# Optimization experiments

Measured on AMD Instinct MI355X. Metric: run time of the kernel, lower is better.

## Reference

```python
import jax, jax.numpy as jnp
import numpy as np

F_SIZE = 256
N_HEAD = 4
D_HEAD = F_SIZE // N_HEAD
B = 16384
E = 31  # number of 'other' entities


def setup_inputs() -> dict:
    key = jax.random.key(0)
    ks = jax.random.split(key, 9)
    s = 1.0 / np.sqrt(F_SIZE)  # ~ nn.Linear init scale
    inp = {
        "ego": jax.random.normal(ks[0], (B, 1, F_SIZE), dtype=jnp.float32),
        "others": jax.random.normal(ks[1], (B, E, F_SIZE), dtype=jnp.float32),
        "mask": jax.random.randint(ks[2], (B, E + 1), 0, 2).astype(bool),
        "Wq": jax.random.uniform(ks[3], (F_SIZE, F_SIZE), jnp.float32, -s, s),
        "Wk": jax.random.uniform(ks[4], (F_SIZE, F_SIZE), jnp.float32, -s, s),
        "Wv": jax.random.uniform(ks[5], (F_SIZE, F_SIZE), jnp.float32, -s, s),
        "Wok": jax.random.uniform(ks[6], (F_SIZE, F_SIZE), jnp.float32, -s, s),
        "Wov": jax.random.uniform(ks[7], (F_SIZE, F_SIZE), jnp.float32, -s, s),
        "Wc": jax.random.uniform(ks[8], (F_SIZE, F_SIZE), jnp.float32, -s, s),
    }
    return inp


def reference(ego, others, mask, Wq, Wk, Wv, Wok, Wov, Wc):
    b = others.shape[0]
    e = others.shape[1]
    # nn.Linear(bias=False): y = x @ W.T
    ego_q = (ego @ Wq.T).reshape(b, 1, N_HEAD, D_HEAD)
    ego_k = (ego @ Wk.T).reshape(b, 1, N_HEAD, D_HEAD)
    ego_v = (ego @ Wv.T).reshape(b, 1, N_HEAD, D_HEAD)
    oth_k = (others @ Wok.T).reshape(b, e, N_HEAD, D_HEAD)
    oth_v = (others @ Wov.T).reshape(b, e, N_HEAD, D_HEAD)
    all_k = jnp.concatenate([ego_k, oth_k], axis=1)  # (b, e+1, h, d)
    all_v = jnp.concatenate([ego_v, oth_v], axis=1)
    # scores: single query per head -> (b, h, 1, e+1)
    scores = jnp.einsum('bqhd,bkhd->bhqk', ego_q, all_k) / np.sqrt(D_HEAD)
    scores = jnp.where(mask[:, None, None, :], jnp.float32(-1e9), scores)
    attn = jax.nn.softmax(scores, axis=-1)
    value = jnp.einsum('bhqk,bkhd->bqhd', attn, all_v).reshape(b, F_SIZE)
    res = ((value @ Wc.T) + ego[:, 0, :]) * 0.5
    return res, attn
```

## Files before the change

kernel.cpp:

```cpp
#include <hip/hip_runtime.h>
#include <hip/hip_bf16.h>

typedef __attribute__((ext_vector_type(8))) short bf16x8;
typedef __attribute__((ext_vector_type(4))) float f32x4;

#define NB 16384
#define NE 31

static __device__ __forceinline__ unsigned short f2b(float f) {
  unsigned int u = __builtin_bit_cast(unsigned int, f);
  return (unsigned short)((u + 0x7fffu + ((u >> 16) & 1u)) >> 16);
}
static __device__ __forceinline__ float b2f(unsigned short h) {
  return __builtin_bit_cast(float, ((unsigned int)h) << 16);
}
static __device__ __forceinline__ unsigned int cvtpk(float a, float b) {
  unsigned int r;
  asm("v_cvt_pk_bf16_f32 %0, %1, %2" : "=v"(r) : "v"(a), "v"(b));
  return r;
}

__global__ void k0_all(const float* __restrict__ wq, const float* __restrict__ wk,
                       const float* __restrict__ wv, const float* __restrict__ wok,
                       const float* __restrict__ wov, const float* __restrict__ wc,
                       unsigned short* __restrict__ W1, unsigned short* __restrict__ W2) {
  int r = blockIdx.x, k = threadIdx.x;
  if (r < 1024) {
    if (r < 256) {
      W1[r * 256 + k] = f2b(0.125f * wq[r * 256 + k]);
    } else if (r < 512) {
      W1[r * 256 + k] = f2b(wk[(r - 256) * 256 + k]);
    } else if (r < 768) {
      W1[r * 256 + k] = f2b(wv[(r - 512) * 256 + k]);
    } else {
      int n = r - 768;
      W2[n * 1280 + 1024 + k] = f2b(wc[n * 256 + k]);
    }
  } else if (r < 2048) {
    int m = r - 1024;
    int h = m >> 8, c = m & 255;
    float acc = 0.f;
#pragma unroll 8
    for (int d = 0; d < 64; ++d)
      acc = fmaf(wq[(h * 64 + d) * 256 + k], wok[(h * 64 + d) * 256 + c], acc);
    W1[(768 + m) * 256 + k] = f2b(0.125f * acc);
  } else {
    int n = r - 2048;
#pragma unroll 1
    for (int mi = 0; mi < 4; ++mi) {
      float acc = 0.f;
#pragma unroll 8
      for (int d = 0; d < 64; ++d)
        acc = fmaf(wov[(mi * 64 + d) * 256 + k], wc[n * 256 + mi * 64 + d], acc);
      W2[n * 1280 + mi * 256 + k] = f2b(acc);
    }
  }
}

__global__ __launch_bounds__(256, 2)
void k1b(const float* __restrict__ ego, const unsigned short* __restrict__ W1,
         unsigned short* __restrict__ qkv2) {
  __shared__ __align__(16) unsigned short Al[64 * 256];
  const int tid = threadIdx.x;
  const int bM = (blockIdx.x >> 1) * 64;
  const int half = (blockIdx.x & 1) * 896;
#pragma unroll
  for (int it = 0; it < 8; ++it) {
    int c = tid + it * 256;
    int row = c >> 5, k8 = c & 31;
    const float4* g = (const float4*)(ego + (size_t)(bM + row) * 256 + k8 * 8);
    float4 x = g[0], y = g[1];
    float t[8] = {x.x, x.y, x.z, x.w, y.x, y.y, y.z, y.w};
    bf16x8 v;
#pragma unroll
    for (int j = 0; j < 8; ++j) v[j] = (short)f2b(t[j]);
    int byteoff = row * 512 + ((k8 * 16) ^ ((row & 7) << 4));
    *(bf16x8*)((char*)Al + byteoff) = v;
  }
  __syncthreads();
  const int w = tid >> 6, lane = tid & 63, lr = lane & 15, lkg = lane >> 4;
#pragma unroll 1
  for (int cb = 0; cb < 7; ++cb) {
    int bN = half + w * 224 + cb * 32;
    f32x4 acc[4][2];
#pragma unroll
    for (int mt = 0; mt < 4; ++mt)
#pragma unroll
      for (int nt = 0; nt < 2; ++nt) acc[mt][nt] = (f32x4){0.f, 0.f, 0.f, 0.f};
#pragma unroll
    for (int kk = 0; kk < 8; ++kk) {
      int kidx = kk * 32 + lkg * 8;
      bf16x8 bfr[2];
#pragma unroll
      for (int nt = 0; nt < 2; ++nt)
        bfr[nt] = *(const bf16x8*)(W1 + (size_t)(bN + nt * 16 + lr) * 256 + kidx);
#pragma unroll
      for (int mt = 0; mt < 4; ++mt) {
        int row = mt * 16 + lr;
        int byteoff = row * 512 + ((kidx * 2) ^ ((row & 7) << 4));
        bf16x8 a = *(const bf16x8*)((const char*)Al + byteoff);
#pragma unroll
        for (int nt = 0; nt < 2; ++nt)
          acc[mt][nt] = __builtin_amdgcn_mfma_f32_16x16x32_bf16(a, bfr[nt], acc[mt][nt], 0, 0, 0);
      }
    }
#pragma unroll
    for (int mt = 0; mt < 4; ++mt)
#pragma unroll
      for (int nt = 0; nt < 2; ++nt)
#pragma unroll
        for (int j = 0; j < 4; ++j) {
          int row = bM + mt * 16 + lkg * 4 + j;
          int col = bN + nt * 16 + lr;
          qkv2[(size_t)row * 1792 + col] = f2b(acc[mt][nt][j]);
        }
  }
}

__global__ __launch_bounds__(64, 4)
void ks_attn(const float* __restrict__ others, const int* __restrict__ mask,
             const unsigned short* __restrict__ qkv2,
             unsigned short* __restrict__ u,
             float* __restrict__ attnout) {
  __shared__ __align__(16) unsigned short Xs[8192];
  const int lane = threadIdx.x;
  const int lr = lane & 15, lkg = lane >> 4;
  const size_t b = blockIdx.x;
  char* Xc = (char*)Xs;
  const unsigned short* qk = qkv2 + b * 1792;

  bf16x8 af[8];
#pragma unroll
  for (int kk = 0; kk < 8; ++kk)
    af[kk] = *(const bf16x8*)(qk + 768 + (lr & 3) * 256 + kk * 32 + lkg * 8);
  ushort4 qa = *(const ushort4*)(qk + lkg * 64 + lr * 4);
  ushort4 kb = *(const ushort4*)(qk + 256 + lkg * 64 + lr * 4);
  ushort4 ve = *(const ushort4*)(qk + 512 + lane * 4);
  int mk0 = mask[b * 32 + 1 + lr];
  int mk1 = (lr == 15) ? 1 : mask[b * 32 + 17 + lr];
  int mkE = mask[b * 32];

  {
    const char* src = (const char*)(others + b * (NE * 256)) + lane * 16;
#pragma unroll
    for (int j = 0; j < NE; ++j) {
      float4 f = *(const float4*)(src + j * 1024);
      uint2 v;
      v.x = cvtpk(f.x, f.y);
      v.y = cvtpk(f.z, f.w);
      *(uint2*)(Xc + j * 512 + ((lane * 8) ^ ((j & 15) << 4))) = v;
    }
    uint2 z; z.x = 0; z.y = 0;
    *(uint2*)(Xc + 31 * 512 + ((lane * 8) ^ ((31 & 15) << 4))) = z;
  }

  float s0p = b2f(qa.x) * b2f(kb.x) + b2f(qa.y) * b2f(kb.y) +
              b2f(qa.z) * b2f(kb.z) + b2f(qa.w) * b2f(kb.w);
#pragma unroll
  for (int off = 1; off < 16; off <<= 1) s0p += __shfl_xor(s0p, off, 16);
  float s0h[4];
  s0h[0] = __shfl(s0p, 0);
  s0h[1] = __shfl(s0p, 16);
  s0h[2] = __shfl(s0p, 32);
  s0h[3] = __shfl(s0p, 48);

  asm volatile("s_waitcnt lgkmcnt(0)" ::: "memory");
  __builtin_amdgcn_sched_barrier(0);

  f32x4 acc0 = (f32x4){0.f, 0.f, 0.f, 0.f};
  f32x4 acc1 = (f32x4){0.f, 0.f, 0.f, 0.f};
#pragma unroll
  for (int kk = 0; kk < 8; ++kk) {
    int co = kk * 64 + lkg * 16;
    bf16x8 b0 = *(const bf16x8*)(Xc + lr * 512 + (co ^ (lr << 4)));
    bf16x8 b1 = *(const bf16x8*)(Xc + (16 + lr) * 512 + (co ^ (lr << 4)));
    acc0 = __builtin_amdgcn_mfma_f32_16x16x32_bf16(af[kk], b0, acc0, 0, 0, 0);
    acc1 = __builtin_amdgcn_mfma_f32_16x16x32_bf16(af[kk], b1, acc1, 0, 0, 0);
  }

  float pr0[4], pr1[4], p0v[4];
#pragma unroll
  for (int j = 0; j < 4; ++j) {
    float sj0 = mk0 ? -1e9f : acc0[j];
    float sj1 = mk1 ? -1e9f : acc1[j];
    float se  = mkE ? -1e9f : s0h[j];
    float mx = fmaxf(se, fmaxf(sj0, sj1));
#pragma unroll
    for (int off = 1; off < 16; off <<= 1) mx = fmaxf(mx, __shfl_xor(mx, off, 16));
    float e0 = __expf(sj0 - mx), e1 = __expf(sj1 - mx), ee = __expf(se - mx);
    float sm = e0 + e1;
#pragma unroll
    for (int off = 1; off < 16; off <<= 1) sm += __shfl_xor(sm, off, 16);
    float rinv = 1.f / (sm + ee);
    pr0[j] = e0 * rinv;
    pr1[j] = e1 * rinv;
    p0v[j] = ee * rinv;
  }
  if (lkg == 0) {
#pragma unroll
    for (int j = 0; j < 4; ++j) {
      attnout[b * 128 + j * 32 + 1 + lr] = pr0[j];
      if (lr < 15) attnout[b * 128 + j * 32 + 17 + lr] = pr1[j];
      if (lr == 0) attnout[b * 128 + j * 32] = p0v[j];
    }
  }

  f32x4 cx[4];
#pragma unroll
  for (int h = 0; h < 4; ++h) cx[h] = (f32x4){0.f, 0.f, 0.f, 0.f};
#pragma unroll
  for (int e = 0; e < NE; ++e) {
    float p0, p1, p2, p3;
    if (e < 16) {
      p0 = __shfl(pr0[0], e); p1 = __shfl(pr0[1], e);
      p2 = __shfl(pr0[2], e); p3 = __shfl(pr0[3], e);
    } else {
      p0 = __shfl(pr1[0], e - 16); p1 = __shfl(pr1[1], e - 16);
      p2 = __shfl(pr1[2], e - 16); p3 = __shfl(pr1[3], e - 16);
    }
    ushort4 xr = *(const ushort4*)(Xc + e * 512 + ((lane * 8) ^ ((e & 15) << 4)));
    float x0 = b2f(xr.x), x1 = b2f(xr.y), x2 = b2f(xr.z), x3 = b2f(xr.w);
    cx[0][0] = fmaf(p0, x0, cx[0][0]); cx[0][1] = fmaf(p0, x1, cx[0][1]);
    cx[0][2] = fmaf(p0, x2, cx[0][2]); cx[0][3] = fmaf(p0, x3, cx[0][3]);
    cx[1][0] = fmaf(p1, x0, cx[1][0]); cx[1][1] = fmaf(p1, x1, cx[1][1]);
    cx[1][2] = fmaf(p1, x2, cx[1][2]); cx[1][3] = fmaf(p1, x3, cx[1][3]);
    cx[2][0] = fmaf(p2, x0, cx[2][0]); cx[2][1] = fmaf(p2, x1, cx[2][1]);
    cx[2][2] = fmaf(p2, x2, cx[2][2]); cx[2][3] = fmaf(p2, x3, cx[2][3]);
    cx[3][0] = fmaf(p3, x0, cx[3][0]); cx[3][1] = fmaf(p3, x1, cx[3][1]);
    cx[3][2] = fmaf(p3, x2, cx[3][2]); cx[3][3] = fmaf(p3, x3, cx[3][3]);
  }
#pragma unroll
  for (int h = 0; h < 4; ++h) {
    ushort4 st;
    st.x = f2b(cx[h][0]); st.y = f2b(cx[h][1]);
    st.z = f2b(cx[h][2]); st.w = f2b(cx[h][3]);
    *(ushort4*)(u + b * 1280 + h * 256 + lane * 4) = st;
  }
  {
    float p0h = (lkg == 0) ? p0v[0] : (lkg == 1) ? p0v[1] : (lkg == 2) ? p0v[2] : p0v[3];
    ushort4 sv;
    sv.x = f2b(p0h * b2f(ve.x)); sv.y = f2b(p0h * b2f(ve.y));
    sv.z = f2b(p0h * b2f(ve.z)); sv.w = f2b(p0h * b2f(ve.w));
    *(ushort4*)(u + b * 1280 + 1024 + lane * 4) = sv;
  }
}

__global__ __launch_bounds__(256, 2)
void k4_out(const unsigned short* __restrict__ u, const unsigned short* __restrict__ W2,
            const float* __restrict__ ego, float* __restrict__ out) {
  __shared__ __align__(16) unsigned short Au[32 * 256];
  const int tid = threadIdx.x;
  const int bM = blockIdx.x * 32;
  const int w = tid >> 6, lane = tid & 63, lr = lane & 15, lkg = lane >> 4;
  f32x4 acc[2][4];
#pragma unroll
  for (int mt = 0; mt < 2; ++mt)
#pragma unroll
    for (int nt = 0; nt < 4; ++nt) acc[mt][nt] = (f32x4){0.f, 0.f, 0.f, 0.f};
#pragma unroll 1
  for (int kc = 0; kc < 5; ++kc) {
#pragma unroll
    for (int it = 0; it < 4; ++it) {
      int c = tid + it * 256;
      int row = c >> 5, k8 = c & 31;
      bf16x8 v = *(const bf16x8*)(u + (size_t)(bM + row) * 1280 + kc * 256 + k8 * 8);
      int byteoff = row * 512 + ((k8 * 16) ^ ((row & 7) << 4));
      *(bf16x8*)((char*)Au + byteoff) = v;
    }
    __syncthreads();
#pragma unroll
    for (int kk = 0; kk < 8; ++kk) {
      int kidx = kk * 32 + lkg * 8;
      bf16x8 bfr[4];
#pragma unroll
      for (int nt = 0; nt < 4; ++nt)
        bfr[nt] = *(const bf16x8*)(W2 + (size_t)(w * 64 + nt * 16 + lr) * 1280 + kc * 256 + kidx);
#pragma unroll
      for (int mt = 0; mt < 2; ++mt) {
        int row = mt * 16 + lr;
        int byteoff = row * 512 + ((kidx * 2) ^ ((row & 7) << 4));
        bf16x8 a = *(const bf16x8*)((const char*)Au + byteoff);
#pragma unroll
        for (int nt = 0; nt < 4; ++nt)
          acc[mt][nt] = __builtin_amdgcn_mfma_f32_16x16x32_bf16(a, bfr[nt], acc[mt][nt], 0, 0, 0);
      }
    }
    __syncthreads();
  }
#pragma unroll
  for (int mt = 0; mt < 2; ++mt)
#pragma unroll
    for (int nt = 0; nt < 4; ++nt)
#pragma unroll
      for (int j = 0; j < 4; ++j) {
        int row = bM + mt * 16 + lkg * 4 + j;
        int col = w * 64 + nt * 16 + lr;
        out[(size_t)row * 256 + col] = (acc[mt][nt][j] + ego[(size_t)row * 256 + col]) * 0.5f;
      }
}

extern "C" void kernel_launch(void* const* d_in, const int* in_sizes, int n_in,
                              void* d_out, int out_size, void* d_ws, size_t ws_size,
                              hipStream_t stream) {
  const float* ego    = (const float*)d_in[0];
  const float* others = (const float*)d_in[1];
  const int*   mask   = (const int*)d_in[2];
  const float* wq  = (const float*)d_in[3];
  const float* wk  = (const float*)d_in[4];
  const float* wv  = (const float*)d_in[5];
  const float* wok = (const float*)d_in[6];
  const float* wov = (const float*)d_in[7];
  const float* wc  = (const float*)d_in[8];

  unsigned short* W1   = (unsigned short*)d_ws;
  unsigned short* W2   = W1 + 1792 * 256;
  unsigned short* qkv2 = W2 + 256 * 1280;
  unsigned short* u    = qkv2 + (size_t)NB * 1792;

  float* res  = (float*)d_out;
  float* attn = res + (size_t)NB * 256;

  hipLaunchKernelGGL(k0_all, dim3(2304), dim3(256), 0, stream,
                     wq, wk, wv, wok, wov, wc, W1, W2);
  hipLaunchKernelGGL(k1b,    dim3(512),  dim3(256), 0, stream, ego, W1, qkv2);
  hipLaunchKernelGGL(ks_attn, dim3(NB), dim3(64), 0, stream,
                     others, mask, qkv2, u, attn);
  hipLaunchKernelGGL(k4_out, dim3(512),  dim3(256), 0, stream, u, W2, ego, res);
}
```

Before: 229.9 us.

## Load GEMM A-fragments straight into registers instead of staging through LDS

In the ego projection GEMM, each wave now loads its ego rows from global memory directly into MFMA A-fragment registers, packing them with v_cvt_pk_bf16_f32. This removes the swizzled LDS tile and its barrier. The output GEMM likewise reads u fragments straight from global memory and drops the per-chunk LDS staging and syncs. The attention kernel's launch bound is relaxed from 4 to 2 blocks per CU, giving it more registers. The trade-off is that all four waves now read the same A rows redundantly from global memory/cache, and the larger register footprint may lower occupancy.

```diff
diff --git a/kernel.cpp b/kernel.cpp
--- a/kernel.cpp
+++ b/kernel.cpp
@@ -18,6 +18,14 @@
   unsigned int r;
   asm("v_cvt_pk_bf16_f32 %0, %1, %2" : "=v"(r) : "v"(a), "v"(b));
   return r;
+}
+static __device__ __forceinline__ bf16x8 pack8(float4 x, float4 y) {
+  int4 t;
+  t.x = (int)cvtpk(x.x, x.y);
+  t.y = (int)cvtpk(x.z, x.w);
+  t.z = (int)cvtpk(y.x, y.y);
+  t.w = (int)cvtpk(y.z, y.w);
+  return __builtin_bit_cast(bf16x8, t);
 }
 
 __global__ void k0_all(const float* __restrict__ wq, const float* __restrict__ wk,
@@ -60,25 +68,23 @@
 __global__ __launch_bounds__(256, 2)
 void k1b(const float* __restrict__ ego, const unsigned short* __restrict__ W1,
          unsigned short* __restrict__ qkv2) {
-  __shared__ __align__(16) unsigned short Al[64 * 256];
   const int tid = threadIdx.x;
   const int bM = (blockIdx.x >> 1) * 64;
   const int half = (blockIdx.x & 1) * 896;
-#pragma unroll
-  for (int it = 0; it < 8; ++it) {
-    int c = tid + it * 256;
-    int row = c >> 5, k8 = c & 31;
-    const float4* g = (const float4*)(ego + (size_t)(bM + row) * 256 + k8 * 8);
-    float4 x = g[0], y = g[1];
-    float t[8] = {x.x, x.y, x.z, x.w, y.x, y.y, y.z, y.w};
-    bf16x8 v;
-#pragma unroll
-    for (int j = 0; j < 8; ++j) v[j] = (short)f2b(t[j]);
-    int byteoff = row * 512 + ((k8 * 16) ^ ((row & 7) << 4));
-    *(bf16x8*)((char*)Al + byteoff) = v;
-  }
-  __syncthreads();
   const int w = tid >> 6, lane = tid & 63, lr = lane & 15, lkg = lane >> 4;
+
+  bf16x8 af[4][8];
+#pragma unroll
+  for (int mt = 0; mt < 4; ++mt) {
+    const float* rowp = ego + (size_t)(bM + mt * 16 + lr) * 256 + lkg * 8;
+#pragma unroll
+    for (int kk = 0; kk < 8; ++kk) {
+      float4 x = *(const float4*)(rowp + kk * 32);
+      float4 y = *(const float4*)(rowp + kk * 32 + 4);
+      af[mt][kk] = pack8(x, y);
+    }
+  }
+
 #pragma unroll 1
   for (int cb = 0; cb < 7; ++cb) {
     int bN = half + w * 224 + cb * 32;
@@ -95,14 +101,10 @@
       for (int nt = 0; nt < 2; ++nt)
         bfr[nt] = *(const bf16x8*)(W1 + (size_t)(bN + nt * 16 + lr) * 256 + kidx);
 #pragma unroll
-      for (int mt = 0; mt < 4; ++mt) {
-        int row = mt * 16 + lr;
-        int byteoff = row * 512 + ((kidx * 2) ^ ((row & 7) << 4));
-        bf16x8 a = *(const bf16x8*)((const char*)Al + byteoff);
+      for (int mt = 0; mt < 4; ++mt)
 #pragma unroll
         for (int nt = 0; nt < 2; ++nt)
-          acc[mt][nt] = __builtin_amdgcn_mfma_f32_16x16x32_bf16(a, bfr[nt], acc[mt][nt], 0, 0, 0);
-      }
+          acc[mt][nt] = __builtin_amdgcn_mfma_f32_16x16x32_bf16(af[mt][kk], bfr[nt], acc[mt][nt], 0, 0, 0);
     }
 #pragma unroll
     for (int mt = 0; mt < 4; ++mt)
@@ -117,7 +119,7 @@
   }
 }
 
-__global__ __launch_bounds__(64, 4)
+__global__ __launch_bounds__(64, 2)
 void ks_attn(const float* __restrict__ others, const int* __restrict__ mask,
              const unsigned short* __restrict__ qkv2,
              unsigned short* __restrict__ u,
@@ -248,7 +250,6 @@
 __global__ __launch_bounds__(256, 2)
 void k4_out(const unsigned short* __restrict__ u, const unsigned short* __restrict__ W2,
             const float* __restrict__ ego, float* __restrict__ out) {
-  __shared__ __align__(16) unsigned short Au[32 * 256];
   const int tid = threadIdx.x;
   const int bM = blockIdx.x * 32;
   const int w = tid >> 6, lane = tid & 63, lr = lane & 15, lkg = lane >> 4;
@@ -260,32 +261,21 @@
 #pragma unroll 1
   for (int kc = 0; kc < 5; ++kc) {
 #pragma unroll
-    for (int it = 0; it < 4; ++it) {
-      int c = tid + it * 256;
-      int row = c >> 5, k8 = c & 31;
-      bf16x8 v = *(const bf16x8*)(u + (size_t)(bM + row) * 1280 + kc * 256 + k8 * 8);
-      int byteoff = row * 512 + ((k8 * 16) ^ ((row & 7) << 4));
-      *(bf16x8*)((char*)Au + byteoff) = v;
-    }
-    __syncthreads();
-#pragma unroll
     for (int kk = 0; kk < 8; ++kk) {
-      int kidx = kk * 32 + lkg * 8;
-      bf16x8 bfr[4];
+      int kidx = kc * 256 + kk * 32 + lkg * 8;
+      bf16x8 a[2], bfr[4];
+#pragma unroll
+      for (int mt = 0; mt < 2; ++mt)
+        a[mt] = *(const bf16x8*)(u + (size_t)(bM + mt * 16 + lr) * 1280 + kidx);
 #pragma unroll
       for (int nt = 0; nt < 4; ++nt)
-        bfr[nt] = *(const bf16x8*)(W2 + (size_t)(w * 64 + nt * 16 + lr) * 1280 + kc * 256 + kidx);
-#pragma unroll
-      for (int mt = 0; mt < 2; ++mt) {
-        int row = mt * 16 + lr;
-        int byteoff = row * 512 + ((kidx * 2) ^ ((row & 7) << 4));
-        bf16x8 a = *(const bf16x8*)((const char*)Au + byteoff);
+        bfr[nt] = *(const bf16x8*)(W2 + (size_t)(w * 64 + nt * 16 + lr) * 1280 + kidx);
+#pragma unroll
+      for (int mt = 0; mt < 2; ++mt)
 #pragma unroll
         for (int nt = 0; nt < 4; ++nt)
-          acc[mt][nt] = __builtin_amdgcn_mfma_f32_16x16x32_bf16(a, bfr[nt], acc[mt][nt], 0, 0, 0);
-      }
-    }
-    __syncthreads();
+          acc[mt][nt] = __builtin_amdgcn_mfma_f32_16x16x32_bf16(a[mt], bfr[nt], acc[mt][nt], 0, 0, 0);
+    }
   }
 #pragma unroll
   for (int mt = 0; mt < 2; ++mt)
```

Measured after the change: 257.8 us. 12.2% more time.
